# Kernel optimization log

Hardware: AMD Instinct MI355X
Metric: run time of the kernel (lower is better)

The kernel has to match this reference:

```python
import jax, jax.numpy as jnp
import numpy as np

N, E, IN, H, HEADS, L, OUT = 4096, 262144, 64, 128, 4, 2, 2
DH = H // HEADS  # 32, per-head dim for both GAT and global MHA
BN_EPS = 1e-5
NEG_SLOPE = 0.2  # GATConv leaky_relu default


def setup_inputs() -> dict:
    key = jax.random.key(0)
    ks = iter(jax.random.split(key, 32))
    rn = lambda shape, s: jax.random.normal(next(ks), shape, jnp.float32) * s
    return {
        "x": rn((N, IN), 1.0),
        "edge_index": jax.random.randint(next(ks), (2, E), 0, N),
        "w_in": rn((H, IN), IN ** -0.5),
        "b_in": rn((H,), 0.02),
        "w_gat": rn((L, H, H), H ** -0.5),
        "att_src": rn((L, HEADS, DH), 0.1),
        "att_dst": rn((L, HEADS, DH), 0.1),
        "b_gat": rn((L, H), 0.02),
        "w_qkv": rn((L, 3 * H, H), H ** -0.5),
        "b_qkv": rn((L, 3 * H), 0.02),
        "w_o": rn((L, H, H), H ** -0.5),
        "b_o": rn((L, H), 0.02),
        "bn_gamma": 1.0 + rn((L, 3, H), 0.05),
        "bn_beta": rn((L, 3, H), 0.05),
        "w1": rn((L, 2 * H, H), H ** -0.5),
        "b1": rn((L, 2 * H), 0.02),
        "w2": rn((L, H, 2 * H), (2 * H) ** -0.5),
        "b2": rn((L, H), 0.02),
        "w_out": rn((OUT, H), H ** -0.5),
        "b_out": rn((OUT,), 0.02),
    }


def _bn(h, g, b):
    # eval-mode BatchNorm1d with running_mean=0, running_var=1
    return h * (g / jnp.sqrt(1.0 + BN_EPS)) + b


def _gat(x, src, dst, w, a_src, a_dst, bias):
    # GATConv(hidden, hidden//heads, heads=HEADS, add_self_loops=False), concat=True
    xp = (x @ w.T).reshape(N, HEADS, DH)                  # [N, HEADS, DH]
    al_s = jnp.einsum('nhd,hd->nh', xp, a_src)            # [N, HEADS]
    al_d = jnp.einsum('nhd,hd->nh', xp, a_dst)
    logit = al_s[src] + al_d[dst]                         # [E, HEADS]
    logit = jnp.where(logit >= 0, logit, NEG_SLOPE * logit)
    m = jax.ops.segment_max(logit, dst, num_segments=N)   # scatter-softmax over dst
    m = jnp.where(jnp.isfinite(m), m, 0.0)
    e = jnp.exp(logit - m[dst])
    denom = jax.ops.segment_sum(e, dst, num_segments=N)
    alpha = e / (denom[dst] + 1e-16)
    out = jax.ops.segment_sum(alpha[:, :, None] * xp[src], dst, num_segments=N)
    return out.reshape(N, H) + bias


def _mha(x, wqkv, bqkv, wo, bo):
    # torch.nn.MultiheadAttention self-attention over all N nodes (one graph)
    qkv = x @ wqkv.T + bqkv
    q, k, v = jnp.split(qkv, 3, axis=-1)
    q = q.reshape(N, HEADS, DH)
    k = k.reshape(N, HEADS, DH)
    v = v.reshape(N, HEADS, DH)
    scores = jnp.einsum('nhd,mhd->hnm', q, k) / jnp.sqrt(jnp.float32(DH))
    attn = jax.nn.softmax(scores, axis=-1)
    out = jnp.einsum('hnm,mhd->nhd', attn, v).reshape(N, H)
    return out @ wo.T + bo


def reference(x, edge_index, w_in, b_in, w_gat, att_src, att_dst, b_gat,
              w_qkv, b_qkv, w_o, b_o, bn_gamma, bn_beta,
              w1, b1, w2, b2, w_out, b_out):
    src, dst = edge_index[0], edge_index[1]
    h = jax.nn.relu(x @ w_in.T + b_in)
    for l in range(L):
        # GPSConv: local GAT branch (dropout inactive in eval)
        h_loc = _gat(h, src, dst, w_gat[l], att_src[l], att_dst[l], b_gat[l]) + h
        h_loc = _bn(h_loc, bn_gamma[l, 0], bn_beta[l, 0])
        # GPSConv: global attention branch
        h_att = _mha(h, w_qkv[l], b_qkv[l], w_o[l], b_o[l]) + h
        h_att = _bn(h_att, bn_gamma[l, 1], bn_beta[l, 1])
        out = h_loc + h_att
        mlp = jax.nn.relu(out @ w1[l].T + b1[l]) @ w2[l].T + b2[l]
        out = _bn(out + mlp, bn_gamma[l, 2], bn_beta[l, 2])
        # GPSRiskModel residual + relu (dropout inactive in eval)
        h = jax.nn.relu(out + h)
    return h @ w_out.T + b_out
```

## Files before the change

kernel.cpp:

```cpp
#include <hip/hip_runtime.h>

#define NN 4096
#define EE 262144
#define INF_ 64
#define HH 128
#define HEADS 4
#define DH 32
#define LL 2
#define NH (NN * HH)
#define KSPLIT 8
#define L2E 1.4426950408889634f

typedef unsigned short u16;
typedef unsigned int u32;
using bf16x8 = __attribute__((ext_vector_type(8))) short;
using f32x4 = __attribute__((ext_vector_type(4))) float;

__device__ __forceinline__ float bf2f(u16 v) { return __uint_as_float(((u32)v) << 16); }
__device__ __forceinline__ u16 f2bf(float f) {
    u32 u = __float_as_uint(f);
    u32 r = (u + 0x7fffu + ((u >> 16) & 1u)) >> 16;
    return (u16)r;
}
__device__ __forceinline__ u32 encf(float f) {
    u32 b = __float_as_uint(f);
    return (b & 0x80000000u) ? ~b : (b | 0x80000000u);
}
__device__ __forceinline__ float decf(u32 u) {
    u32 b = (u & 0x80000000u) ? (u & 0x7fffffffu) : ~u;
    return __uint_as_float(b);
}

__global__ __launch_bounds__(256) void k_detect(const u16* __restrict__ x, int* __restrict__ flag,
                                                int* __restrict__ cnt, u32* __restrict__ gmax) {
    int t = threadIdx.x;
    for (int i = t; i < NN; i += 256) cnt[i] = 0;
    if (t < 16) gmax[t] = 0;
    __shared__ int cs[256];
    u16 v = x[2 * t];
    int e = (v >> 7) & 0xFF;
    cs[t] = (e >= 100 && e <= 140) ? 1 : 0;
    __syncthreads();
    for (int s = 128; s > 0; s >>= 1) {
        if (t < s) cs[t] += cs[t + s];
        __syncthreads();
    }
    if (t == 0) *flag = (cs[0] >= 128) ? 1 : 0;
}

#define MAXSEG 16
struct SegF { const void* src[MAXSEG]; int dst[MAXSEG]; int n[MAXSEG]; int cnt; };
__global__ void k_cvtf(SegF S, float* __restrict__ W, const int* __restrict__ flag) {
    int seg = blockIdx.y;
    if (seg >= S.cnt) return;
    int n = S.n[seg];
    float* d = W + S.dst[seg];
    const void* s = S.src[seg];
    int f = *flag;
    for (int i = blockIdx.x * 256 + threadIdx.x; i < n; i += gridDim.x * 256)
        d[i] = f ? bf2f(((const u16*)s)[i]) : ((const float*)s)[i];
}
struct SegB { const void* src[8]; u16* dst[8]; u16* dst2[8]; int n[8]; int cnt; };
__global__ void k_cvtb(SegB S, const int* __restrict__ flag) {
    int seg = blockIdx.y;
    if (seg >= S.cnt) return;
    int f = *flag;
    u16* d = S.dst[seg];
    u16* d2 = S.dst2[seg];
    if (f && !d2) return;
    int n = S.n[seg];
    const void* s = S.src[seg];
    for (int i = blockIdx.x * 256 + threadIdx.x; i < n; i += gridDim.x * 256) {
        if (d2) {
            float v = f ? bf2f(((const u16*)s)[i]) : ((const float*)s)[i];
            u16 h = f2bf(v);
            d[i] = h;
            d2[i] = f2bf(v - bf2f(h));
        } else {
            d[i] = f2bf(((const float*)s)[i]);
        }
    }
}

__global__ void k_hist(const int* __restrict__ dst, int* __restrict__ cnt) {
    int e = blockIdx.x * blockDim.x + threadIdx.x;
    if (e < EE) atomicAdd(&cnt[dst[e]], 1);
}
__global__ __launch_bounds__(256) void k_scan(const int* __restrict__ cnt, int* __restrict__ rowstart,
                                              int* __restrict__ cursor) {
    __shared__ int part[256];
    int t = threadIdx.x;
    int loc[16];
    int s = 0;
#pragma unroll
    for (int i = 0; i < 16; ++i) { loc[i] = s; s += cnt[t * 16 + i]; }
    part[t] = s;
    __syncthreads();
    for (int off = 1; off < 256; off <<= 1) {
        int v = part[t];
        int a = (t >= off) ? part[t - off] : 0;
        __syncthreads();
        part[t] = v + a;
        __syncthreads();
    }
    int base = (t == 0) ? 0 : part[t - 1];
#pragma unroll
    for (int i = 0; i < 16; ++i) {
        rowstart[t * 16 + i] = base + loc[i];
        cursor[t * 16 + i] = base + loc[i];
    }
}
__global__ void k_scatter(const int* __restrict__ src, const int* __restrict__ dst,
                          int* __restrict__ cursor, int* __restrict__ esrc) {
    int e = blockIdx.x * blockDim.x + threadIdx.x;
    if (e < EE) {
        int d = dst[e];
        int p = atomicAdd(&cursor[d], 1);
        esrc[p] = src[e];
    }
}

__global__ __launch_bounds__(128) void k_mgemm(const u16* __restrict__ Ahi, const u16* __restrict__ Alo,
                                               const u16* __restrict__ Wc, const u16* __restrict__ Wd,
                                               const int* __restrict__ flag,
                                               const float* __restrict__ bias,
                                               float* __restrict__ outf, u16* __restrict__ outb16,
                                               u16* __restrict__ outhi, u16* __restrict__ outlo,
                                               int K, int J, int relu) {
    const u16* Wb = (*flag) ? Wd : Wc;
    int wave = threadIdx.x >> 6, lane = threadIdx.x & 63;
    int grp = lane >> 4, lcol = lane & 15;
    int m0 = blockIdx.x * 32 + wave * 16;
    int j0 = blockIdx.y * 64;
    f32x4 acc[4];
#pragma unroll
    for (int s = 0; s < 4; ++s) acc[s] = (f32x4){0.f, 0.f, 0.f, 0.f};
    const u16* ah = Ahi + (size_t)(m0 + lcol) * K + grp * 8;
    const u16* al = Alo + (size_t)(m0 + lcol) * K + grp * 8;
    const u16* wb = Wb + (size_t)(j0 + lcol) * K + grp * 8;
    for (int k = 0; k < K; k += 32) {
        bf16x8 va = *(const bf16x8*)(ah + k);
        bf16x8 vl = *(const bf16x8*)(al + k);
#pragma unroll
        for (int s = 0; s < 4; ++s) {
            bf16x8 vw = *(const bf16x8*)(wb + (size_t)s * 16 * K + k);
            acc[s] = __builtin_amdgcn_mfma_f32_16x16x32_bf16(va, vw, acc[s], 0, 0, 0);
            acc[s] = __builtin_amdgcn_mfma_f32_16x16x32_bf16(vl, vw, acc[s], 0, 0, 0);
        }
    }
#pragma unroll
    for (int s = 0; s < 4; ++s) {
        int col = j0 + s * 16 + lcol;
        float bs = bias ? bias[col] : 0.f;
#pragma unroll
        for (int r = 0; r < 4; ++r) {
            float v = acc[s][r] + bs;
            if (relu) v = fmaxf(v, 0.f);
            size_t idx = (size_t)(m0 + grp * 4 + r) * J + col;
            if (outf) outf[idx] = v;
            if (outb16) outb16[idx] = f2bf(v);
            if (outhi) {
                u16 hv = f2bf(v);
                outhi[idx] = hv;
                outlo[idx] = f2bf(v - bf2f(hv));
            }
        }
    }
}

__global__ __launch_bounds__(128) void k_gemm_gq(const u16* __restrict__ Ahi, const u16* __restrict__ Alo,
                                                 const u16* __restrict__ wgatc, const u16* __restrict__ wgatd,
                                                 const u16* __restrict__ wqkvc, const u16* __restrict__ wqkvd,
                                                 const int* __restrict__ flag,
                                                 const float* __restrict__ bqkv,
                                                 u16* __restrict__ xpb, u16* __restrict__ qkvb) {
    int wave = threadIdx.x >> 6, lane = threadIdx.x & 63;
    int grp = lane >> 4, lcol = lane & 15;
    int m0 = blockIdx.x * 32 + wave * 16;
    int jb = blockIdx.y;
    int j0 = jb * 64;
    int f = *flag;
    const u16* wgat = f ? wgatd : wgatc;
    const u16* wqkv = f ? wqkvd : wqkvc;
    const u16* Wb = (jb < 2) ? (wgat + (size_t)j0 * HH) : (wqkv + (size_t)(j0 - 128) * HH);
    f32x4 acc[4];
#pragma unroll
    for (int s = 0; s < 4; ++s) acc[s] = (f32x4){0.f, 0.f, 0.f, 0.f};
    const u16* ah = Ahi + (size_t)(m0 + lcol) * HH + grp * 8;
    const u16* al = Alo + (size_t)(m0 + lcol) * HH + grp * 8;
    const u16* wb = Wb + (size_t)lcol * HH + grp * 8;
    for (int k = 0; k < HH; k += 32) {
        bf16x8 va = *(const bf16x8*)(ah + k);
        bf16x8 vl = *(const bf16x8*)(al + k);
#pragma unroll
        for (int s = 0; s < 4; ++s) {
            bf16x8 vw = *(const bf16x8*)(wb + (size_t)s * 16 * HH + k);
            acc[s] = __builtin_amdgcn_mfma_f32_16x16x32_bf16(va, vw, acc[s], 0, 0, 0);
            acc[s] = __builtin_amdgcn_mfma_f32_16x16x32_bf16(vl, vw, acc[s], 0, 0, 0);
        }
    }
    if (jb < 2) {
#pragma unroll
        for (int s = 0; s < 4; ++s) {
            int col = j0 + s * 16 + lcol;
#pragma unroll
            for (int r = 0; r < 4; ++r)
                xpb[(size_t)(m0 + grp * 4 + r) * HH + col] = f2bf(acc[s][r]);
        }
    } else {
#pragma unroll
        for (int s = 0; s < 4; ++s) {
            int colq = j0 - 128 + s * 16 + lcol;
            float bs = bqkv[colq];
#pragma unroll
            for (int r = 0; r < 4; ++r)
                qkvb[(size_t)(m0 + grp * 4 + r) * 384 + colq] = f2bf(acc[s][r] + bs);
        }
    }
}

__global__ __launch_bounds__(256) void k_attlog(const u16* __restrict__ xpb, const float* __restrict__ asrc,
                                                const float* __restrict__ adst, float* __restrict__ als,
                                                float* __restrict__ ald, u32* __restrict__ gmax) {
    int t = blockIdx.x * 256 + threadIdx.x;
    int n = t >> 2, hh = t & 3;
    const u16* xr = xpb + (size_t)n * HH + hh * DH;
    float s1 = 0.f, s2 = 0.f;
#pragma unroll
    for (int d = 0; d < DH; ++d) {
        float v = bf2f(xr[d]);
        s1 += v * asrc[hh * DH + d];
        s2 += v * adst[hh * DH + d];
    }
    als[t] = s1;
    ald[t] = s2;
    __shared__ float red[256];
    int lt = threadIdx.x;
    red[lt] = s1;
    __syncthreads();
    for (int off = 128; off >= 4; off >>= 1) {
        if (lt < off) red[lt] = fmaxf(red[lt], red[lt + off]);
        __syncthreads();
    }
    if (lt < 4) atomicMax(&gmax[lt], encf(red[lt]));
    __syncthreads();
    red[lt] = s2;
    __syncthreads();
    for (int off = 128; off >= 4; off >>= 1) {
        if (lt < off) red[lt] = fmaxf(red[lt], red[lt + off]);
        __syncthreads();
    }
    if (lt < 4) atomicMax(&gmax[4 + lt], encf(red[lt]));
}

__global__ __launch_bounds__(128) void k_gemm_wo(const u16* __restrict__ Ahi, const u16* __restrict__ Alo,
                                                 const u16* __restrict__ Wc, const u16* __restrict__ Wd,
                                                 const int* __restrict__ flag,
                                                 const float* __restrict__ bias,
                                                 const float* __restrict__ gatb, const float* __restrict__ hbuf,
                                                 const float* __restrict__ bgat, const float* __restrict__ gam,
                                                 const float* __restrict__ bet,
                                                 float* __restrict__ outb, u16* __restrict__ ohi,
                                                 u16* __restrict__ olo) {
    const u16* Wb = (*flag) ? Wd : Wc;
    int wave = threadIdx.x >> 6, lane = threadIdx.x & 63;
    int grp = lane >> 4, lcol = lane & 15;
    int m0 = blockIdx.x * 32 + wave * 16;
    int j0 = blockIdx.y * 64;
    f32x4 acc[4];
#pragma unroll
    for (int s = 0; s < 4; ++s) acc[s] = (f32x4){0.f, 0.f, 0.f, 0.f};
    const u16* ah = Ahi + (size_t)(m0 + lcol) * HH + grp * 8;
    const u16* al = Alo + (size_t)(m0 + lcol) * HH + grp * 8;
    const u16* wb = Wb + (size_t)(j0 + lcol) * HH + grp * 8;
    for (int k = 0; k < HH; k += 32) {
        bf16x8 va = *(const bf16x8*)(ah + k);
        bf16x8 vl = *(const bf16x8*)(al + k);
#pragma unroll
        for (int s = 0; s < 4; ++s) {
            bf16x8 vw = *(const bf16x8*)(wb + (size_t)s * 16 * HH + k);
            acc[s] = __builtin_amdgcn_mfma_f32_16x16x32_bf16(va, vw, acc[s], 0, 0, 0);
            acc[s] = __builtin_amdgcn_mfma_f32_16x16x32_bf16(vl, vw, acc[s], 0, 0, 0);
        }
    }
    float rs = rsqrtf(1.00001f);
#pragma unroll
    for (int s = 0; s < 4; ++s) {
        int col = j0 + s * 16 + lcol;
        float bs = bias[col];
        float g0 = gam[col] * rs, b0 = bet[col];
        float g1 = gam[HH + col] * rs, b1 = bet[HH + col];
        float bg = bgat[col];
#pragma unroll
        for (int r = 0; r < 4; ++r) {
            size_t idx = (size_t)(m0 + grp * 4 + r) * HH + col;
            float proj = acc[s][r] + bs;
            float hv = hbuf[idx];
            float hl = g0 * (gatb[idx] + bg + hv) + b0;
            float ha = g1 * (proj + hv) + b1;
            float v = hl + ha;
            outb[idx] = v;
            u16 hb = f2bf(v);
            ohi[idx] = hb;
            olo[idx] = f2bf(v - bf2f(hb));
        }
    }
}

__global__ __launch_bounds__(128) void k_gemm_w2(const u16* __restrict__ Ahi, const u16* __restrict__ Alo,
                                                 const u16* __restrict__ Wc, const u16* __restrict__ Wd,
                                                 const int* __restrict__ flag,
                                                 const float* __restrict__ bias,
                                                 const float* __restrict__ outb, const float* __restrict__ gam2,
                                                 const float* __restrict__ bet2,
                                                 float* __restrict__ hbuf, u16* __restrict__ hhi,
                                                 u16* __restrict__ hlo) {
    const u16* Wb = (*flag) ? Wd : Wc;
    int wave = threadIdx.x >> 6, lane = threadIdx.x & 63;
    int grp = lane >> 4, lcol = lane & 15;
    int m0 = blockIdx.x * 32 + wave * 16;
    int j0 = blockIdx.y * 64;
    const int K = 2 * HH;
    f32x4 acc[4];
#pragma unroll
    for (int s = 0; s < 4; ++s) acc[s] = (f32x4){0.f, 0.f, 0.f, 0.f};
    const u16* ah = Ahi + (size_t)(m0 + lcol) * K + grp * 8;
    const u16* al = Alo + (size_t)(m0 + lcol) * K + grp * 8;
    const u16* wb = Wb + (size_t)(j0 + lcol) * K + grp * 8;
    for (int k = 0; k < K; k += 32) {
        bf16x8 va = *(const bf16x8*)(ah + k);
        bf16x8 vl = *(const bf16x8*)(al + k);
#pragma unroll
        for (int s = 0; s < 4; ++s) {
            bf16x8 vw = *(const bf16x8*)(wb + (size_t)s * 16 * K + k);
            acc[s] = __builtin_amdgcn_mfma_f32_16x16x32_bf16(va, vw, acc[s], 0, 0, 0);
            acc[s] = __builtin_amdgcn_mfma_f32_16x16x32_bf16(vl, vw, acc[s], 0, 0, 0);
        }
    }
    float rs = rsqrtf(1.00001f);
#pragma unroll
    for (int s = 0; s < 4; ++s) {
        int col = j0 + s * 16 + lcol;
        float bs = bias[col];
        float g2 = gam2[col] * rs, b2 = bet2[col];
#pragma unroll
        for (int r = 0; r < 4; ++r) {
            size_t idx = (size_t)(m0 + grp * 4 + r) * HH + col;
            float mlpo = acc[s][r] + bs;
            float o2 = g2 * (outb[idx] + mlpo) + b2;
            float v = fmaxf(o2 + hbuf[idx], 0.f);
            hbuf[idx] = v;
            u16 hb = f2bf(v);
            hhi[idx] = hb;
            hlo[idx] = f2bf(v - bf2f(hb));
        }
    }
}

#define GCHUNK 256
__global__ __launch_bounds__(128) void k_gat_node(const int* __restrict__ esrc, const int* __restrict__ rowstart,
                                                  const int* __restrict__ cnt, const float* __restrict__ als,
                                                  const float* __restrict__ ald, const u16* __restrict__ xpb,
                                                  float* __restrict__ gatout, const u32* __restrict__ gmax) {
    int n = blockIdx.x, t = threadIdx.x;
    int base = rowstart[n], c = cnt[n];
    float4 adv = ((const float4*)ald)[n];
    float ad[4] = {adv.x, adv.y, adv.z, adv.w};
    float M2[4];
#pragma unroll
    for (int h = 0; h < 4; ++h) {
        float bound = decf(gmax[h]) + decf(gmax[4 + h]);
        float M = bound >= 0.f ? bound : 0.2f * bound;
        M2[h] = M * L2E;
    }
    __shared__ float red[512];
    __shared__ float elds[GCHUNK * 4];
    __shared__ int slds[GCHUNK];
    float dsum[4] = {0.f, 0.f, 0.f, 0.f};
    float acc = 0.f;
    int ht = t >> 5;
    for (int ch = 0; ch < c; ch += GCHUNK) {
        int cn = min(GCHUNK, c - ch);
        __syncthreads();
        for (int i = t; i < cn; i += 128) {
            int s = esrc[base + ch + i];
            slds[i] = s;
            float4 as = ((const float4*)als)[s];
            float lg, e;
            lg = as.x + ad[0]; lg = lg >= 0.f ? lg : 0.2f * lg; e = __builtin_exp2f(lg * L2E - M2[0]); elds[i * 4 + 0] = e; dsum[0] += e;
            lg = as.y + ad[1]; lg = lg >= 0.f ? lg : 0.2f * lg; e = __builtin_exp2f(lg * L2E - M2[1]); elds[i * 4 + 1] = e; dsum[1] += e;
            lg = as.z + ad[2]; lg = lg >= 0.f ? lg : 0.2f * lg; e = __builtin_exp2f(lg * L2E - M2[2]); elds[i * 4 + 2] = e; dsum[2] += e;
            lg = as.w + ad[3]; lg = lg >= 0.f ? lg : 0.2f * lg; e = __builtin_exp2f(lg * L2E - M2[3]); elds[i * 4 + 3] = e; dsum[3] += e;
        }
        __syncthreads();
        int i = 0;
        for (; i + 4 <= cn; i += 4) {
            int s0 = slds[i], s1 = slds[i + 1], s2 = slds[i + 2], s3 = slds[i + 3];
            float x0 = bf2f(xpb[(size_t)s0 * HH + t]);
            float x1 = bf2f(xpb[(size_t)s1 * HH + t]);
            float x2 = bf2f(xpb[(size_t)s2 * HH + t]);
            float x3 = bf2f(xpb[(size_t)s3 * HH + t]);
            acc += elds[i * 4 + ht] * x0 + elds[(i + 1) * 4 + ht] * x1;
            acc += elds[(i + 2) * 4 + ht] * x2 + elds[(i + 3) * 4 + ht] * x3;
        }
        for (; i < cn; ++i) acc += elds[i * 4 + ht] * bf2f(xpb[(size_t)slds[i] * HH + t]);
    }
    __syncthreads();
#pragma unroll
    for (int h = 0; h < 4; ++h) red[h * 128 + t] = dsum[h];
    __syncthreads();
    for (int s2 = 64; s2 > 0; s2 >>= 1) {
        if (t < s2) {
#pragma unroll
            for (int h = 0; h < 4; ++h)
                red[h * 128 + t] += red[h * 128 + t + s2];
        }
        __syncthreads();
    }
    float inv = 1.f / (red[ht * 128] + 1e-16f);
    gatout[(size_t)n * HH + t] = acc * inv;
}

__global__ __launch_bounds__(256) void k_mha_split(const u16* __restrict__ qkvb,
                                                   float* __restrict__ PM, float* __restrict__ PL,
                                                   u16* __restrict__ PO) {
    const float C1 = 0.17677669529663687f * L2E;
    int head = blockIdx.x & 3;
    int qt = (blockIdx.x >> 2) & 31;
    int ks = blockIdx.x >> 7;
    int tid = threadIdx.x;
    int wave = tid >> 6, lane = tid & 63;
    int grp = lane >> 4, lcol = lane & 15;

    __shared__ __align__(16) u16 Klds[64][40];
    __shared__ __align__(16) u32 Vlds[32][36];
    __shared__ __align__(16) u16 Plds[4][32][66];

    int qrow0 = qt * 128 + wave * 32;
    bf16x8 aQ0 = *(const bf16x8*)(qkvb + (size_t)(qrow0 + lcol) * 384 + head * 32 + grp * 8);
    bf16x8 aQ1 = *(const bf16x8*)(qkvb + (size_t)(qrow0 + 16 + lcol) * 384 + head * 32 + grp * 8);

    short onev = (lcol == 0) ? (short)0x3F80 : (short)0;
    bf16x8 bOne = {onev, onev, onev, onev, onev, onev, onev, onev};

    f32x4 oc00 = {0.f, 0.f, 0.f, 0.f}, oc01 = {0.f, 0.f, 0.f, 0.f};
    f32x4 oc10 = {0.f, 0.f, 0.f, 0.f}, oc11 = {0.f, 0.f, 0.f, 0.f};
    f32x4 ol0 = {0.f, 0.f, 0.f, 0.f}, ol1 = {0.f, 0.f, 0.f, 0.f};
    float msh = -INFINITY;

    int isK = (tid < 128);
    int st = tid & 127;
    int skey = st >> 1, shalf = (st & 1) * 16;
    int vj = st & 31, dgrp = st >> 5;
    int vkey0 = 32 * (vj & 1) + (vj >> 1);
    const u16* kptr = qkvb + 128 + head * 32 + shalf;
    const u16* vptr = qkvb + 256 + head * 32 + dgrp * 8;

    int kt0 = ks * (NN / KSPLIT);
    bf16x8 r0, r1;
    if (isK) {
        r0 = *(const bf16x8*)(kptr + (size_t)(kt0 + skey) * 384);
        r1 = *(const bf16x8*)(kptr + (size_t)(kt0 + skey) * 384 + 8);
    } else {
        r0 = *(const bf16x8*)(vptr + (size_t)(kt0 + vkey0) * 384);
        r1 = *(const bf16x8*)(vptr + (size_t)(kt0 + vkey0 + 16) * 384);
    }

    const int NT = (NN / KSPLIT) / 64;
    for (int t = 0; t < NT; ++t) {
        if (isK) {
            *(bf16x8*)(&Klds[skey][shalf]) = r0;
            *(bf16x8*)(&Klds[skey][shalf + 8]) = r1;
        } else {
#pragma unroll
            for (int j = 0; j < 8; ++j)
                Vlds[dgrp * 8 + j][vj] = (u32)(u16)r0[j] | ((u32)(u16)r1[j] << 16);
        }
        __syncthreads();
        if (t + 1 < NT) {
            int kn = kt0 + (t + 1) * 64;
            if (isK) {
                r0 = *(const bf16x8*)(kptr + (size_t)(kn + skey) * 384);
                r1 = *(const bf16x8*)(kptr + (size_t)(kn + skey) * 384 + 8);
            } else {
                r0 = *(const bf16x8*)(vptr + (size_t)(kn + vkey0) * 384);
                r1 = *(const bf16x8*)(vptr + (size_t)(kn + vkey0 + 16) * 384);
            }
        }
        f32x4 sc0[4], sc1[4];
        f32x4 zero = {0.f, 0.f, 0.f, 0.f};
#pragma unroll
        for (int s = 0; s < 4; ++s) {
            bf16x8 bK = *(const bf16x8*)(&Klds[s * 16 + lcol][grp * 8]);
            sc0[s] = __builtin_amdgcn_mfma_f32_16x16x32_bf16(aQ0, bK, zero, 0, 0, 0);
            sc1[s] = __builtin_amdgcn_mfma_f32_16x16x32_bf16(aQ1, bK, zero, 0, 0, 0);
        }
        float mymax = sc0[0][0];
#pragma unroll
        for (int s = 0; s < 4; ++s)
#pragma unroll
            for (int r = 0; r < 4; ++r) {
                mymax = fmaxf(mymax, sc0[s][r]);
                mymax = fmaxf(mymax, sc1[s][r]);
            }
        mymax = fmaxf(mymax, __shfl_xor(mymax, 1));
        mymax = fmaxf(mymax, __shfl_xor(mymax, 2));
        mymax = fmaxf(mymax, __shfl_xor(mymax, 4));
        mymax = fmaxf(mymax, __shfl_xor(mymax, 8));
        float mnew = fmaxf(msh, mymax * C1);
        float cc = __builtin_exp2f(msh - mnew);
        msh = mnew;
#pragma unroll
        for (int r = 0; r < 4; ++r) {
            float p0 = __builtin_exp2f(__builtin_fmaf(sc0[0][r], C1, -mnew));
            float p1 = __builtin_exp2f(__builtin_fmaf(sc0[1][r], C1, -mnew));
            float p2 = __builtin_exp2f(__builtin_fmaf(sc0[2][r], C1, -mnew));
            float p3 = __builtin_exp2f(__builtin_fmaf(sc0[3][r], C1, -mnew));
            u32 a01 = __builtin_amdgcn_perm(__float_as_uint(p1), __float_as_uint(p0), 0x07060302u);
            u32 a23 = __builtin_amdgcn_perm(__float_as_uint(p3), __float_as_uint(p2), 0x07060302u);
            *(uint2*)(&Plds[wave][grp * 4 + r][4 * lcol]) = make_uint2(a01, a23);
            float q0 = __builtin_exp2f(__builtin_fmaf(sc1[0][r], C1, -mnew));
            float q1 = __builtin_exp2f(__builtin_fmaf(sc1[1][r], C1, -mnew));
            float q2 = __builtin_exp2f(__builtin_fmaf(sc1[2][r], C1, -mnew));
            float q3 = __builtin_exp2f(__builtin_fmaf(sc1[3][r], C1, -mnew));
            u32 b01 = __builtin_amdgcn_perm(__float_as_uint(q1), __float_as_uint(q0), 0x07060302u);
            u32 b23 = __builtin_amdgcn_perm(__float_as_uint(q3), __float_as_uint(q2), 0x07060302u);
            *(uint2*)(&Plds[wave][16 + grp * 4 + r][4 * lcol]) = make_uint2(b01, b23);
        }
        oc00 *= cc; oc01 *= cc; ol0 *= cc;
        oc10 *= cc; oc11 *= cc; ol1 *= cc;
#pragma unroll
        for (int c2 = 0; c2 < 2; ++c2) {
            bf16x8 aP0 = *(const bf16x8*)(&Plds[wave][lcol][c2 * 32 + grp * 8]);
            bf16x8 aP1 = *(const bf16x8*)(&Plds[wave][16 + lcol][c2 * 32 + grp * 8]);
            bf16x8 bV0 = *(const bf16x8*)(&Vlds[lcol][c2 * 16 + grp * 4]);
            bf16x8 bV1 = *(const bf16x8*)(&Vlds[16 + lcol][c2 * 16 + grp * 4]);
            oc00 = __builtin_amdgcn_mfma_f32_16x16x32_bf16(aP0, bV0, oc00, 0, 0, 0);
            oc01 = __builtin_amdgcn_mfma_f32_16x16x32_bf16(aP0, bV1, oc01, 0, 0, 0);
            ol0 = __builtin_amdgcn_mfma_f32_16x16x32_bf16(aP0, bOne, ol0, 0, 0, 0);
            oc10 = __builtin_amdgcn_mfma_f32_16x16x32_bf16(aP1, bV0, oc10, 0, 0, 0);
            oc11 = __builtin_amdgcn_mfma_f32_16x16x32_bf16(aP1, bV1, oc11, 0, 0, 0);
            ol1 = __builtin_amdgcn_mfma_f32_16x16x32_bf16(aP1, bOne, ol1, 0, 0, 0);
        }
        __syncthreads();
    }
#pragma unroll
    for (int r = 0; r < 4; ++r) {
        int row0 = qrow0 + grp * 4 + r;
        size_t b0 = ((size_t)row0 * HEADS + head) * KSPLIT + ks;
        PO[b0 * 32 + lcol] = f2bf(oc00[r]);
        PO[b0 * 32 + 16 + lcol] = f2bf(oc01[r]);
        int row1 = row0 + 16;
        size_t b1 = ((size_t)row1 * HEADS + head) * KSPLIT + ks;
        PO[b1 * 32 + lcol] = f2bf(oc10[r]);
        PO[b1 * 32 + 16 + lcol] = f2bf(oc11[r]);
        if (lcol == 0) {
            PM[b0] = msh;
            PL[b0] = ol0[r];
            PM[b1] = msh;
            PL[b1] = ol1[r];
        }
    }
}

__global__ void k_mha_comb(const float* __restrict__ PM, const float* __restrict__ PL,
                           const u16* __restrict__ PO, u16* __restrict__ atthi,
                           u16* __restrict__ attlo) {
    int t = blockIdx.x * 256 + threadIdx.x;
    if (t >= NN * HH) return;
    int row = t >> 7, col = t & 127;
    int head = col >> 5, dim = col & 31;
    size_t b0 = ((size_t)row * HEADS + head) * KSPLIT;
    float m = -INFINITY;
#pragma unroll
    for (int k = 0; k < KSPLIT; ++k) m = fmaxf(m, PM[b0 + k]);
    float l = 0.f, o = 0.f;
#pragma unroll
    for (int k = 0; k < KSPLIT; ++k) {
        float w = __builtin_exp2f(PM[b0 + k] - m);
        l += PL[b0 + k] * w;
        o += bf2f(PO[(b0 + k) * 32 + dim]) * w;
    }
    float v = o / l;
    u16 h = f2bf(v);
    atthi[t] = h;
    attlo[t] = f2bf(v - bf2f(h));
}

__global__ __launch_bounds__(64) void k_out(const float* __restrict__ h, const float* __restrict__ w,
                                            const float* __restrict__ b, void* __restrict__ yout,
                                            const int* __restrict__ flag) {
    int n = blockIdx.x, l = threadIdx.x;
    float a0 = 0.f, a1 = 0.f;
    for (int k = l; k < HH; k += 64) {
        float hv = h[(size_t)n * HH + k];
        a0 += hv * w[k];
        a1 += hv * w[HH + k];
    }
#pragma unroll
    for (int off = 32; off > 0; off >>= 1) {
        a0 += __shfl_xor(a0, off);
        a1 += __shfl_xor(a1, off);
    }
    if (l == 0) {
        float o0 = a0 + b[0], o1 = a1 + b[1];
        if (*flag) {
            u16* y = (u16*)yout;
            y[n * 2 + 0] = f2bf(o0);
            y[n * 2 + 1] = f2bf(o1);
        } else {
            float* y = (float*)yout;
            y[n * 2 + 0] = o0;
            y[n * 2 + 1] = o1;
        }
    }
}

extern "C" void kernel_launch(void* const* d_in, const int* in_sizes, int n_in,
                              void* d_out, int out_size, void* d_ws, size_t ws_size,
                              hipStream_t stream) {
    float* W = (float*)d_ws;
    size_t o = 0;
    auto take = [&](size_t n) { size_t r = o; o += n; return r; };
    size_t pb_in = take(HH);
    size_t pattS = take(LL * HEADS * DH);
    size_t pattD = take(LL * HEADS * DH);
    size_t pb_gat = take(LL * HH);
    size_t pb_qkv = take(LL * 3 * HH);
    size_t pb_o  = take(LL * HH);
    size_t pbn_g = take(LL * 3 * HH);
    size_t pbn_b = take(LL * 3 * HH);
    size_t pb1   = take(LL * 2 * HH);
    size_t pb2   = take(LL * HH);
    size_t pw_out = take(2 * HH);
    size_t pb_out = take(2);
    auto takeb = [&](size_t nu16) { size_t r = o; o += (nu16 + 1) / 2; return r; };
    size_t bw_in  = takeb(HH * INF_);
    size_t bw_gat = takeb(LL * HH * HH);
    size_t bw_qkv = takeb(LL * 3 * HH * HH);
    size_t bw_o   = takeb(LL * HH * HH);
    size_t bw1    = takeb(LL * 2 * HH * HH);
    size_t bw2    = takeb(LL * HH * 2 * HH);
    o = (o + 127) & ~(size_t)127;
    size_t ohbuf = take(NH);
    size_t ogat  = take(NH);
    size_t otmp  = take(NH);
    size_t oals  = take(NN * HEADS);
    size_t oald  = take(NN * HEADS);
    size_t opm   = take(NN * HEADS * KSPLIT);
    size_t opl   = take(NN * HEADS * KSPLIT);
    size_t opo   = takeb((size_t)NN * HEADS * KSPLIT * 32);
    size_t oqkvb = takeb(NN * 384);
    size_t oxpb  = takeb(NH);
    size_t oxhi  = takeb(NN * INF_);
    size_t oxlo  = takeb(NN * INF_);
    size_t ohhi  = takeb(NH);
    size_t ohlo  = takeb(NH);
    size_t oahi  = takeb(NH);
    size_t oalo  = takeb(NH);
    size_t oohi  = takeb(NH);
    size_t oolo  = takeb(NH);
    size_t omhi  = takeb(NN * 2 * HH);
    size_t omlo  = takeb(NN * 2 * HH);
    int* ibase    = (int*)(W + o);
    int* iflag    = ibase;
    int* cnt      = ibase + 64;
    int* rowstart = cnt + NN;
    int* cursor   = rowstart + NN;
    int* esrc     = cursor + NN;
    u32* gmax     = (u32*)(esrc + EE);

    float* hbuf = W + ohbuf;
    float* gatb = W + ogat;
    float* tmp  = W + otmp;
    float* als  = W + oals;
    float* ald  = W + oald;
    float* pmb  = W + opm;
    float* plb  = W + opl;
    u16* pob  = (u16*)(W + opo);
    u16* qkvb = (u16*)(W + oqkvb);
    u16* xpb  = (u16*)(W + oxpb);
    u16* xhi = (u16*)(W + oxhi), *xlo = (u16*)(W + oxlo);
    u16* hhi = (u16*)(W + ohhi), *hlo = (u16*)(W + ohlo);
    u16* ahi = (u16*)(W + oahi), *alo = (u16*)(W + oalo);
    u16* ohi = (u16*)(W + oohi), *olo = (u16*)(W + oolo);
    u16* mhi = (u16*)(W + omhi), *mlo = (u16*)(W + omlo);

    const int* src = (const int*)d_in[1];
    const int* dst = (const int*)d_in[1] + EE;
    const u16* dw_in  = (const u16*)d_in[2];
    const u16* dw_gat = (const u16*)d_in[4];
    const u16* dw_qkv = (const u16*)d_in[8];
    const u16* dw_o   = (const u16*)d_in[10];
    const u16* dw1    = (const u16*)d_in[14];
    const u16* dw2    = (const u16*)d_in[16];

    k_detect<<<1, 256, 0, stream>>>((const u16*)d_in[0], iflag, cnt, gmax);

    SegF SF = {};
    int nf = 0;
    auto addf = [&](int idx, size_t off, int n) { SF.src[nf] = d_in[idx]; SF.dst[nf] = (int)off; SF.n[nf] = n; ++nf; };
    addf(3, pb_in, HH);
    addf(5, pattS, LL * HEADS * DH);
    addf(6, pattD, LL * HEADS * DH);
    addf(7, pb_gat, LL * HH);
    addf(9, pb_qkv, LL * 3 * HH);
    addf(11, pb_o, LL * HH);
    addf(12, pbn_g, LL * 3 * HH);
    addf(13, pbn_b, LL * 3 * HH);
    addf(15, pb1, LL * 2 * HH);
    addf(17, pb2, LL * HH);
    addf(18, pw_out, 2 * HH);
    addf(19, pb_out, 2);
    SF.cnt = nf;
    k_cvtf<<<dim3(8, nf), 256, 0, stream>>>(SF, W, iflag);

    SegB SB = {};
    int nb = 0;
    auto addb = [&](int idx, size_t off, int n, u16* d2) {
        SB.src[nb] = d_in[idx]; SB.dst[nb] = (u16*)(W + off); SB.dst2[nb] = d2; SB.n[nb] = n; ++nb;
    };
    addb(2, bw_in, HH * INF_, nullptr);
    addb(4, bw_gat, LL * HH * HH, nullptr);
    addb(8, bw_qkv, LL * 3 * HH * HH, nullptr);
    addb(10, bw_o, LL * HH * HH, nullptr);
    addb(14, bw1, LL * 2 * HH * HH, nullptr);
    addb(16, bw2, LL * HH * 2 * HH, nullptr);
    SB.src[nb] = d_in[0]; SB.dst[nb] = xhi; SB.dst2[nb] = xlo; SB.n[nb] = NN * INF_; ++nb;
    SB.cnt = nb;
    k_cvtb<<<dim3(128, nb), 256, 0, stream>>>(SB, iflag);

    k_hist<<<EE / 256, 256, 0, stream>>>(dst, cnt);
    k_scan<<<1, 256, 0, stream>>>(cnt, rowstart, cursor);
    k_scatter<<<EE / 256, 256, 0, stream>>>(src, dst, cursor, esrc);

    k_mgemm<<<dim3(NN / 32, HH / 64), 128, 0, stream>>>(xhi, xlo, (u16*)(W + bw_in), dw_in, iflag,
                                                        W + pb_in, hbuf, nullptr, hhi, hlo, INF_, HH, 1);

    for (int l = 0; l < LL; ++l) {
        k_gemm_gq<<<dim3(NN / 32, 8), 128, 0, stream>>>(hhi, hlo,
                                                        (u16*)(W + bw_gat) + (size_t)l * HH * HH,
                                                        dw_gat + (size_t)l * HH * HH,
                                                        (u16*)(W + bw_qkv) + (size_t)l * 3 * HH * HH,
                                                        dw_qkv + (size_t)l * 3 * HH * HH,
                                                        iflag, W + pb_qkv + l * 3 * HH, xpb, qkvb);
        k_attlog<<<(NN * HEADS) / 256, 256, 0, stream>>>(xpb, W + pattS + l * HEADS * DH,
                                                         W + pattD + l * HEADS * DH, als, ald,
                                                         gmax + l * 8);
        k_gat_node<<<NN, 128, 0, stream>>>(esrc, rowstart, cnt, als, ald, xpb, gatb, gmax + l * 8);
        k_mha_split<<<(NN / 128) * HEADS * KSPLIT, 256, 0, stream>>>(qkvb, pmb, plb, pob);
        k_mha_comb<<<(NN * HH) / 256, 256, 0, stream>>>(pmb, plb, pob, ahi, alo);
        k_gemm_wo<<<dim3(NN / 32, HH / 64), 128, 0, stream>>>(ahi, alo,
                                                              (u16*)(W + bw_o) + (size_t)l * HH * HH,
                                                              dw_o + (size_t)l * HH * HH, iflag,
                                                              W + pb_o + l * HH, gatb, hbuf,
                                                              W + pb_gat + l * HH, W + pbn_g + l * 3 * HH,
                                                              W + pbn_b + l * 3 * HH, tmp, ohi, olo);
        k_mgemm<<<dim3(NN / 32, 256 / 64), 128, 0, stream>>>(ohi, olo,
                                                             (u16*)(W + bw1) + (size_t)l * 2 * HH * HH,
                                                             dw1 + (size_t)l * 2 * HH * HH, iflag,
                                                             W + pb1 + l * 2 * HH, nullptr, nullptr,
                                                             mhi, mlo, HH, 2 * HH, 1);
        k_gemm_w2<<<dim3(NN / 32, HH / 64), 128, 0, stream>>>(mhi, mlo,
                                                              (u16*)(W + bw2) + (size_t)l * HH * 2 * HH,
                                                              dw2 + (size_t)l * HH * 2 * HH, iflag,
                                                              W + pb2 + l * HH, tmp,
                                                              W + pbn_g + l * 3 * HH + 2 * HH,
                                                              W + pbn_b + l * 3 * HH + 2 * HH,
                                                              hbuf, hhi, hlo);
    }
    k_out<<<NN, 64, 0, stream>>>(hbuf, W + pw_out, W + pb_out, d_out, iflag);
}
```

Measured before the change: 324.9 us.

## Fuse GAT aggregation and MHA split kernels into one heterogeneous launch

Merges the per-node GAT aggregation kernel and the split-K flash-attention kernel into a single launch. The first GM blocks run attention and the remaining NN blocks run GAT, sharing memory through a union. The GAT path now uses 256 threads per node, with two halves interleaving edges and a final combine. This removes a launch and lets the gather-bound GAT work overlap the MFMA-bound attention on the GPU. In exchange, the larger union shared memory and 256-thread GAT blocks may lower occupancy or add reduction overhead for small-degree nodes.

```diff
diff --git a/kernel.cpp b/kernel.cpp
--- a/kernel.cpp
+++ b/kernel.cpp
@@ -10,6 +10,7 @@
 #define NH (NN * HH)
 #define KSPLIT 8
 #define L2E 1.4426950408889634f
+#define GM ((NN / 128) * HEADS * KSPLIT)
 
 typedef unsigned short u16;
 typedef unsigned int u32;
@@ -358,207 +359,224 @@
 }
 
 #define GCHUNK 256
-__global__ __launch_bounds__(128) void k_gat_node(const int* __restrict__ esrc, const int* __restrict__ rowstart,
-                                                  const int* __restrict__ cnt, const float* __restrict__ als,
-                                                  const float* __restrict__ ald, const u16* __restrict__ xpb,
-                                                  float* __restrict__ gatout, const u32* __restrict__ gmax) {
-    int n = blockIdx.x, t = threadIdx.x;
-    int base = rowstart[n], c = cnt[n];
-    float4 adv = ((const float4*)ald)[n];
-    float ad[4] = {adv.x, adv.y, adv.z, adv.w};
-    float M2[4];
-#pragma unroll
-    for (int h = 0; h < 4; ++h) {
-        float bound = decf(gmax[h]) + decf(gmax[4 + h]);
-        float M = bound >= 0.f ? bound : 0.2f * bound;
-        M2[h] = M * L2E;
-    }
-    __shared__ float red[512];
-    __shared__ float elds[GCHUNK * 4];
-    __shared__ int slds[GCHUNK];
-    float dsum[4] = {0.f, 0.f, 0.f, 0.f};
-    float acc = 0.f;
-    int ht = t >> 5;
-    for (int ch = 0; ch < c; ch += GCHUNK) {
-        int cn = min(GCHUNK, c - ch);
+struct SmemMha {
+    u16 K[64][40];
+    u32 V[32][36];
+    u16 P[4][32][66];
+};
+struct SmemGat {
+    float red4[4 * 256];
+    float accl[256];
+    float elds[GCHUNK * 4];
+    int slds[GCHUNK];
+};
+union SmemU {
+    SmemMha m;
+    SmemGat g;
+};
+
+__global__ __launch_bounds__(256) void k_gat_mha(const u16* __restrict__ qkvb,
+                                                 float* __restrict__ PM, float* __restrict__ PL,
+                                                 u16* __restrict__ PO,
+                                                 const int* __restrict__ esrc, const int* __restrict__ rowstart,
+                                                 const int* __restrict__ cnt, const float* __restrict__ als,
+                                                 const float* __restrict__ ald, const u16* __restrict__ xpb,
+                                                 float* __restrict__ gatout, const u32* __restrict__ gmax) {
+    __shared__ __align__(16) SmemU S;
+    int tid = threadIdx.x;
+    if (blockIdx.x < GM) {
+        const float C1 = 0.17677669529663687f * L2E;
+        int head = blockIdx.x & 3;
+        int qt = (blockIdx.x >> 2) & 31;
+        int ks = blockIdx.x >> 7;
+        int wave = tid >> 6, lane = tid & 63;
+        int grp = lane >> 4, lcol = lane & 15;
+
+        int qrow0 = qt * 128 + wave * 32;
+        bf16x8 aQ0 = *(const bf16x8*)(qkvb + (size_t)(qrow0 + lcol) * 384 + head * 32 + grp * 8);
+        bf16x8 aQ1 = *(const bf16x8*)(qkvb + (size_t)(qrow0 + 16 + lcol) * 384 + head * 32 + grp * 8);
+
+        short onev = (lcol == 0) ? (short)0x3F80 : (short)0;
+        bf16x8 bOne = {onev, onev, onev, onev, onev, onev, onev, onev};
+
+        f32x4 oc00 = {0.f, 0.f, 0.f, 0.f}, oc01 = {0.f, 0.f, 0.f, 0.f};
+        f32x4 oc10 = {0.f, 0.f, 0.f, 0.f}, oc11 = {0.f, 0.f, 0.f, 0.f};
+        f32x4 ol0 = {0.f, 0.f, 0.f, 0.f}, ol1 = {0.f, 0.f, 0.f, 0.f};
+        float msh = -INFINITY;
+
+        int isK = (tid < 128);
+        int st = tid & 127;
+        int skey = st >> 1, shalf = (st & 1) * 16;
+        int vj = st & 31, dgrp = st >> 5;
+        int vkey0 = 32 * (vj & 1) + (vj >> 1);
+        const u16* kptr = qkvb + 128 + head * 32 + shalf;
+        const u16* vptr = qkvb + 256 + head * 32 + dgrp * 8;
+
+        int kt0 = ks * (NN / KSPLIT);
+        bf16x8 r0, r1;
+        if (isK) {
+            r0 = *(const bf16x8*)(kptr + (size_t)(kt0 + skey) * 384);
+            r1 = *(const bf16x8*)(kptr + (size_t)(kt0 + skey) * 384 + 8);
+        } else {
+            r0 = *(const bf16x8*)(vptr + (size_t)(kt0 + vkey0) * 384);
+            r1 = *(const bf16x8*)(vptr + (size_t)(kt0 + vkey0 + 16) * 384);
+        }
+
+        const int NT = (NN / KSPLIT) / 64;
+        for (int t = 0; t < NT; ++t) {
+            if (isK) {
+                *(bf16x8*)(&S.m.K[skey][shalf]) = r0;
+                *(bf16x8*)(&S.m.K[skey][shalf + 8]) = r1;
+            } else {
+#pragma unroll
+                for (int j = 0; j < 8; ++j)
+                    S.m.V[dgrp * 8 + j][vj] = (u32)(u16)r0[j] | ((u32)(u16)r1[j] << 16);
+            }
+            __syncthreads();
+            if (t + 1 < NT) {
+                int kn = kt0 + (t + 1) * 64;
+                if (isK) {
+                    r0 = *(const bf16x8*)(kptr + (size_t)(kn + skey) * 384);
+                    r1 = *(const bf16x8*)(kptr + (size_t)(kn + skey) * 384 + 8);
+                } else {
+                    r0 = *(const bf16x8*)(vptr + (size_t)(kn + vkey0) * 384);
+                    r1 = *(const bf16x8*)(vptr + (size_t)(kn + vkey0 + 16) * 384);
+                }
+            }
+            f32x4 sc0[4], sc1[4];
+            f32x4 zero = {0.f, 0.f, 0.f, 0.f};
+#pragma unroll
+            for (int s = 0; s < 4; ++s) {
+                bf16x8 bK = *(const bf16x8*)(&S.m.K[s * 16 + lcol][grp * 8]);
+                sc0[s] = __builtin_amdgcn_mfma_f32_16x16x32_bf16(aQ0, bK, zero, 0, 0, 0);
+                sc1[s] = __builtin_amdgcn_mfma_f32_16x16x32_bf16(aQ1, bK, zero, 0, 0, 0);
+            }
+            float mymax = sc0[0][0];
+#pragma unroll
+            for (int s = 0; s < 4; ++s)
+#pragma unroll
+                for (int r = 0; r < 4; ++r) {
+                    mymax = fmaxf(mymax, sc0[s][r]);
+                    mymax = fmaxf(mymax, sc1[s][r]);
+                }
+            mymax = fmaxf(mymax, __shfl_xor(mymax, 1));
+            mymax = fmaxf(mymax, __shfl_xor(mymax, 2));
+            mymax = fmaxf(mymax, __shfl_xor(mymax, 4));
+            mymax = fmaxf(mymax, __shfl_xor(mymax, 8));
+            float mnew = fmaxf(msh, mymax * C1);
+            float cc = __builtin_exp2f(msh - mnew);
+            msh = mnew;
+#pragma unroll
+            for (int r = 0; r < 4; ++r) {
+                float p0 = __builtin_exp2f(__builtin_fmaf(sc0[0][r], C1, -mnew));
+                float p1 = __builtin_exp2f(__builtin_fmaf(sc0[1][r], C1, -mnew));
+                float p2 = __builtin_exp2f(__builtin_fmaf(sc0[2][r], C1, -mnew));
+                float p3 = __builtin_exp2f(__builtin_fmaf(sc0[3][r], C1, -mnew));
+                u32 a01 = __builtin_amdgcn_perm(__float_as_uint(p1), __float_as_uint(p0), 0x07060302u);
+                u32 a23 = __builtin_amdgcn_perm(__float_as_uint(p3), __float_as_uint(p2), 0x07060302u);
+                *(uint2*)(&S.m.P[wave][grp * 4 + r][4 * lcol]) = make_uint2(a01, a23);
+                float q0 = __builtin_exp2f(__builtin_fmaf(sc1[0][r], C1, -mnew));
+                float q1 = __builtin_exp2f(__builtin_fmaf(sc1[1][r], C1, -mnew));
+                float q2 = __builtin_exp2f(__builtin_fmaf(sc1[2][r], C1, -mnew));
+                float q3 = __builtin_exp2f(__builtin_fmaf(sc1[3][r], C1, -mnew));
+                u32 b01 = __builtin_amdgcn_perm(__float_as_uint(q1), __float_as_uint(q0), 0x07060302u);
+                u32 b23 = __builtin_amdgcn_perm(__float_as_uint(q3), __float_as_uint(q2), 0x07060302u);
+                *(uint2*)(&S.m.P[wave][16 + grp * 4 + r][4 * lcol]) = make_uint2(b01, b23);
+            }
+            oc00 *= cc; oc01 *= cc; ol0 *= cc;
+            oc10 *= cc; oc11 *= cc; ol1 *= cc;
+#pragma unroll
+            for (int c2 = 0; c2 < 2; ++c2) {
+                bf16x8 aP0 = *(const bf16x8*)(&S.m.P[wave][lcol][c2 * 32 + grp * 8]);
+                bf16x8 aP1 = *(const bf16x8*)(&S.m.P[wave][16 + lcol][c2 * 32 + grp * 8]);
+                bf16x8 bV0 = *(const bf16x8*)(&S.m.V[lcol][c2 * 16 + grp * 4]);
+                bf16x8 bV1 = *(const bf16x8*)(&S.m.V[16 + lcol][c2 * 16 + grp * 4]);
+                oc00 = __builtin_amdgcn_mfma_f32_16x16x32_bf16(aP0, bV0, oc00, 0, 0, 0);
+                oc01 = __builtin_amdgcn_mfma_f32_16x16x32_bf16(aP0, bV1, oc01, 0, 0, 0);
+                ol0 = __builtin_amdgcn_mfma_f32_16x16x32_bf16(aP0, bOne, ol0, 0, 0, 0);
+                oc10 = __builtin_amdgcn_mfma_f32_16x16x32_bf16(aP1, bV0, oc10, 0, 0, 0);
+                oc11 = __builtin_amdgcn_mfma_f32_16x16x32_bf16(aP1, bV1, oc11, 0, 0, 0);
+                ol1 = __builtin_amdgcn_mfma_f32_16x16x32_bf16(aP1, bOne, ol1, 0, 0, 0);
+            }
+            __syncthreads();
+        }
+#pragma unroll
+        for (int r = 0; r < 4; ++r) {
+            int row0 = qrow0 + grp * 4 + r;
+            size_t b0 = ((size_t)row0 * HEADS + head) * KSPLIT + ks;
+            PO[b0 * 32 + lcol] = f2bf(oc00[r]);
+            PO[b0 * 32 + 16 + lcol] = f2bf(oc01[r]);
+            int row1 = row0 + 16;
+            size_t b1 = ((size_t)row1 * HEADS + head) * KSPLIT + ks;
+            PO[b1 * 32 + lcol] = f2bf(oc10[r]);
+            PO[b1 * 32 + 16 + lcol] = f2bf(oc11[r]);
+            if (lcol == 0) {
+                PM[b0] = msh;
+                PL[b0] = ol0[r];
+                PM[b1] = msh;
+                PL[b1] = ol1[r];
+            }
+        }
+    } else {
+        int n = blockIdx.x - GM;
+        int t = tid;
+        int dim = t & 127, half = t >> 7;
+        int base = rowstart[n], c = cnt[n];
+        float4 adv = ((const float4*)ald)[n];
+        float ad[4] = {adv.x, adv.y, adv.z, adv.w};
+        float M2[4];
+#pragma unroll
+        for (int h = 0; h < 4; ++h) {
+            float bound = decf(gmax[h]) + decf(gmax[4 + h]);
+            float M = bound >= 0.f ? bound : 0.2f * bound;
+            M2[h] = M * L2E;
+        }
+        float dsum[4] = {0.f, 0.f, 0.f, 0.f};
+        float acc = 0.f;
+        int ht = dim >> 5;
+        for (int ch = 0; ch < c; ch += GCHUNK) {
+            int cn = min(GCHUNK, c - ch);
+            __syncthreads();
+            for (int i = t; i < cn; i += 256) {
+                int s = esrc[base + ch + i];
+                S.g.slds[i] = s;
+                float4 as = ((const float4*)als)[s];
+                float lg, e;
+                lg = as.x + ad[0]; lg = lg >= 0.f ? lg : 0.2f * lg; e = __builtin_exp2f(lg * L2E - M2[0]); S.g.elds[i * 4 + 0] = e; dsum[0] += e;
+                lg = as.y + ad[1]; lg = lg >= 0.f ? lg : 0.2f * lg; e = __builtin_exp2f(lg * L2E - M2[1]); S.g.elds[i * 4 + 1] = e; dsum[1] += e;
+                lg = as.z + ad[2]; lg = lg >= 0.f ? lg : 0.2f * lg; e = __builtin_exp2f(lg * L2E - M2[2]); S.g.elds[i * 4 + 2] = e; dsum[2] += e;
+                lg = as.w + ad[3]; lg = lg >= 0.f ? lg : 0.2f * lg; e = __builtin_exp2f(lg * L2E - M2[3]); S.g.elds[i * 4 + 3] = e; dsum[3] += e;
+            }
+            __syncthreads();
+            int i = half;
+            for (; i + 6 < cn; i += 8) {
+                int s0 = S.g.slds[i], s1 = S.g.slds[i + 2], s2 = S.g.slds[i + 4], s3 = S.g.slds[i + 6];
+                float x0 = bf2f(xpb[(size_t)s0 * HH + dim]);
+                float x1 = bf2f(xpb[(size_t)s1 * HH + dim]);
+                float x2 = bf2f(xpb[(size_t)s2 * HH + dim]);
+                float x3 = bf2f(xpb[(size_t)s3 * HH + dim]);
+                acc += S.g.elds[i * 4 + ht] * x0 + S.g.elds[(i + 2) * 4 + ht] * x1;
+                acc += S.g.elds[(i + 4) * 4 + ht] * x2 + S.g.elds[(i + 6) * 4 + ht] * x3;
+            }
+            for (; i < cn; i += 2)
+                acc += S.g.elds[i * 4 + ht] * bf2f(xpb[(size_t)S.g.slds[i] * HH + dim]);
+        }
         __syncthreads();
-        for (int i = t; i < cn; i += 128) {
-            int s = esrc[base + ch + i];
-            slds[i] = s;
-            float4 as = ((const float4*)als)[s];
-            float lg, e;
-            lg = as.x + ad[0]; lg = lg >= 0.f ? lg : 0.2f * lg; e = __builtin_exp2f(lg * L2E - M2[0]); elds[i * 4 + 0] = e; dsum[0] += e;
-            lg = as.y + ad[1]; lg = lg >= 0.f ? lg : 0.2f * lg; e = __builtin_exp2f(lg * L2E - M2[1]); elds[i * 4 + 1] = e; dsum[1] += e;
-            lg = as.z + ad[2]; lg = lg >= 0.f ? lg : 0.2f * lg; e = __builtin_exp2f(lg * L2E - M2[2]); elds[i * 4 + 2] = e; dsum[2] += e;
-            lg = as.w + ad[3]; lg = lg >= 0.f ? lg : 0.2f * lg; e = __builtin_exp2f(lg * L2E - M2[3]); elds[i * 4 + 3] = e; dsum[3] += e;
-        }
+#pragma unroll
+        for (int h = 0; h < 4; ++h) S.g.red4[h * 256 + t] = dsum[h];
+        S.g.accl[t] = acc;
         __syncthreads();
-        int i = 0;
-        for (; i + 4 <= cn; i += 4) {
-            int s0 = slds[i], s1 = slds[i + 1], s2 = slds[i + 2], s3 = slds[i + 3];
-            float x0 = bf2f(xpb[(size_t)s0 * HH + t]);
-            float x1 = bf2f(xpb[(size_t)s1 * HH + t]);
-            float x2 = bf2f(xpb[(size_t)s2 * HH + t]);
-            float x3 = bf2f(xpb[(size_t)s3 * HH + t]);
-            acc += elds[i * 4 + ht] * x0 + elds[(i + 1) * 4 + ht] * x1;
-            acc += elds[(i + 2) * 4 + ht] * x2 + elds[(i + 3) * 4 + ht] * x3;
-        }
-        for (; i < cn; ++i) acc += elds[i * 4 + ht] * bf2f(xpb[(size_t)slds[i] * HH + t]);
-    }
-    __syncthreads();
-#pragma unroll
-    for (int h = 0; h < 4; ++h) red[h * 128 + t] = dsum[h];
-    __syncthreads();
-    for (int s2 = 64; s2 > 0; s2 >>= 1) {
-        if (t < s2) {
-#pragma unroll
-            for (int h = 0; h < 4; ++h)
-                red[h * 128 + t] += red[h * 128 + t + s2];
-        }
-        __syncthreads();
-    }
-    float inv = 1.f / (red[ht * 128] + 1e-16f);
-    gatout[(size_t)n * HH + t] = acc * inv;
-}
-
-__global__ __launch_bounds__(256) void k_mha_split(const u16* __restrict__ qkvb,
-                                                   float* __restrict__ PM, float* __restrict__ PL,
-                                                   u16* __restrict__ PO) {
-    const float C1 = 0.17677669529663687f * L2E;
-    int head = blockIdx.x & 3;
-    int qt = (blockIdx.x >> 2) & 31;
-    int ks = blockIdx.x >> 7;
-    int tid = threadIdx.x;
-    int wave = tid >> 6, lane = tid & 63;
-    int grp = lane >> 4, lcol = lane & 15;
-
-    __shared__ __align__(16) u16 Klds[64][40];
-    __shared__ __align__(16) u32 Vlds[32][36];
-    __shared__ __align__(16) u16 Plds[4][32][66];
-
-    int qrow0 = qt * 128 + wave * 32;
-    bf16x8 aQ0 = *(const bf16x8*)(qkvb + (size_t)(qrow0 + lcol) * 384 + head * 32 + grp * 8);
-    bf16x8 aQ1 = *(const bf16x8*)(qkvb + (size_t)(qrow0 + 16 + lcol) * 384 + head * 32 + grp * 8);
-
-    short onev = (lcol == 0) ? (short)0x3F80 : (short)0;
-    bf16x8 bOne = {onev, onev, onev, onev, onev, onev, onev, onev};
-
-    f32x4 oc00 = {0.f, 0.f, 0.f, 0.f}, oc01 = {0.f, 0.f, 0.f, 0.f};
-    f32x4 oc10 = {0.f, 0.f, 0.f, 0.f}, oc11 = {0.f, 0.f, 0.f, 0.f};
-    f32x4 ol0 = {0.f, 0.f, 0.f, 0.f}, ol1 = {0.f, 0.f, 0.f, 0.f};
-    float msh = -INFINITY;
-
-    int isK = (tid < 128);
-    int st = tid & 127;
-    int skey = st >> 1, shalf = (st & 1) * 16;
-    int vj = st & 31, dgrp = st >> 5;
-    int vkey0 = 32 * (vj & 1) + (vj >> 1);
-    const u16* kptr = qkvb + 128 + head * 32 + shalf;
-    const u16* vptr = qkvb + 256 + head * 32 + dgrp * 8;
-
-    int kt0 = ks * (NN / KSPLIT);
-    bf16x8 r0, r1;
-    if (isK) {
-        r0 = *(const bf16x8*)(kptr + (size_t)(kt0 + skey) * 384);
-        r1 = *(const bf16x8*)(kptr + (size_t)(kt0 + skey) * 384 + 8);
-    } else {
-        r0 = *(const bf16x8*)(vptr + (size_t)(kt0 + vkey0) * 384);
-        r1 = *(const bf16x8*)(vptr + (size_t)(kt0 + vkey0 + 16) * 384);
-    }
-
-    const int NT = (NN / KSPLIT) / 64;
-    for (int t = 0; t < NT; ++t) {
-        if (isK) {
-            *(bf16x8*)(&Klds[skey][shalf]) = r0;
-            *(bf16x8*)(&Klds[skey][shalf + 8]) = r1;
-        } else {
-#pragma unroll
-            for (int j = 0; j < 8; ++j)
-                Vlds[dgrp * 8 + j][vj] = (u32)(u16)r0[j] | ((u32)(u16)r1[j] << 16);
-        }
-        __syncthreads();
-        if (t + 1 < NT) {
-            int kn = kt0 + (t + 1) * 64;
-            if (isK) {
-                r0 = *(const bf16x8*)(kptr + (size_t)(kn + skey) * 384);
-                r1 = *(const bf16x8*)(kptr + (size_t)(kn + skey) * 384 + 8);
-            } else {
-                r0 = *(const bf16x8*)(vptr + (size_t)(kn + vkey0) * 384);
-                r1 = *(const bf16x8*)(vptr + (size_t)(kn + vkey0 + 16) * 384);
-            }
-        }
-        f32x4 sc0[4], sc1[4];
-        f32x4 zero = {0.f, 0.f, 0.f, 0.f};
-#pragma unroll
-        for (int s = 0; s < 4; ++s) {
-            bf16x8 bK = *(const bf16x8*)(&Klds[s * 16 + lcol][grp * 8]);
-            sc0[s] = __builtin_amdgcn_mfma_f32_16x16x32_bf16(aQ0, bK, zero, 0, 0, 0);
-            sc1[s] = __builtin_amdgcn_mfma_f32_16x16x32_bf16(aQ1, bK, zero, 0, 0, 0);
-        }
-        float mymax = sc0[0][0];
-#pragma unroll
-        for (int s = 0; s < 4; ++s)
-#pragma unroll
-            for (int r = 0; r < 4; ++r) {
-                mymax = fmaxf(mymax, sc0[s][r]);
-                mymax = fmaxf(mymax, sc1[s][r]);
-            }
-        mymax = fmaxf(mymax, __shfl_xor(mymax, 1));
-        mymax = fmaxf(mymax, __shfl_xor(mymax, 2));
-        mymax = fmaxf(mymax, __shfl_xor(mymax, 4));
-        mymax = fmaxf(mymax, __shfl_xor(mymax, 8));
-        float mnew = fmaxf(msh, mymax * C1);
-        float cc = __builtin_exp2f(msh - mnew);
-        msh = mnew;
-#pragma unroll
-        for (int r = 0; r < 4; ++r) {
-            float p0 = __builtin_exp2f(__builtin_fmaf(sc0[0][r], C1, -mnew));
-            float p1 = __builtin_exp2f(__builtin_fmaf(sc0[1][r], C1, -mnew));
-            float p2 = __builtin_exp2f(__builtin_fmaf(sc0[2][r], C1, -mnew));
-            float p3 = __builtin_exp2f(__builtin_fmaf(sc0[3][r], C1, -mnew));
-            u32 a01 = __builtin_amdgcn_perm(__float_as_uint(p1), __float_as_uint(p0), 0x07060302u);
-            u32 a23 = __builtin_amdgcn_perm(__float_as_uint(p3), __float_as_uint(p2), 0x07060302u);
-            *(uint2*)(&Plds[wave][grp * 4 + r][4 * lcol]) = make_uint2(a01, a23);
-            float q0 = __builtin_exp2f(__builtin_fmaf(sc1[0][r], C1, -mnew));
-            float q1 = __builtin_exp2f(__builtin_fmaf(sc1[1][r], C1, -mnew));
-            float q2 = __builtin_exp2f(__builtin_fmaf(sc1[2][r], C1, -mnew));
-            float q3 = __builtin_exp2f(__builtin_fmaf(sc1[3][r], C1, -mnew));
-            u32 b01 = __builtin_amdgcn_perm(__float_as_uint(q1), __float_as_uint(q0), 0x07060302u);
-            u32 b23 = __builtin_amdgcn_perm(__float_as_uint(q3), __float_as_uint(q2), 0x07060302u);
-            *(uint2*)(&Plds[wave][16 + grp * 4 + r][4 * lcol]) = make_uint2(b01, b23);
-        }
-        oc00 *= cc; oc01 *= cc; ol0 *= cc;
-        oc10 *= cc; oc11 *= cc; ol1 *= cc;
-#pragma unroll
-        for (int c2 = 0; c2 < 2; ++c2) {
-            bf16x8 aP0 = *(const bf16x8*)(&Plds[wave][lcol][c2 * 32 + grp * 8]);
-            bf16x8 aP1 = *(const bf16x8*)(&Plds[wave][16 + lcol][c2 * 32 + grp * 8]);
-            bf16x8 bV0 = *(const bf16x8*)(&Vlds[lcol][c2 * 16 + grp * 4]);
-            bf16x8 bV1 = *(const bf16x8*)(&Vlds[16 + lcol][c2 * 16 + grp * 4]);
-            oc00 = __builtin_amdgcn_mfma_f32_16x16x32_bf16(aP0, bV0, oc00, 0, 0, 0);
-            oc01 = __builtin_amdgcn_mfma_f32_16x16x32_bf16(aP0, bV1, oc01, 0, 0, 0);
-            ol0 = __builtin_amdgcn_mfma_f32_16x16x32_bf16(aP0, bOne, ol0, 0, 0, 0);
-            oc10 = __builtin_amdgcn_mfma_f32_16x16x32_bf16(aP1, bV0, oc10, 0, 0, 0);
-            oc11 = __builtin_amdgcn_mfma_f32_16x16x32_bf16(aP1, bV1, oc11, 0, 0, 0);
-            ol1 = __builtin_amdgcn_mfma_f32_16x16x32_bf16(aP1, bOne, ol1, 0, 0, 0);
-        }
-        __syncthreads();
-    }
-#pragma unroll
-    for (int r = 0; r < 4; ++r) {
-        int row0 = qrow0 + grp * 4 + r;
-        size_t b0 = ((size_t)row0 * HEADS + head) * KSPLIT + ks;
-        PO[b0 * 32 + lcol] = f2bf(oc00[r]);
-        PO[b0 * 32 + 16 + lcol] = f2bf(oc01[r]);
-        int row1 = row0 + 16;
-        size_t b1 = ((size_t)row1 * HEADS + head) * KSPLIT + ks;
-        PO[b1 * 32 + lcol] = f2bf(oc10[r]);
-        PO[b1 * 32 + 16 + lcol] = f2bf(oc11[r]);
-        if (lcol == 0) {
-            PM[b0] = msh;
-            PL[b0] = ol0[r];
-            PM[b1] = msh;
-            PL[b1] = ol1[r];
+        for (int s2 = 128; s2 > 0; s2 >>= 1) {
+            if (t < s2) {
+#pragma unroll
+                for (int h = 0; h < 4; ++h)
+                    S.g.red4[h * 256 + t] += S.g.red4[h * 256 + t + s2];
+            }
+            __syncthreads();
+        }
+        if (t < 128) {
+            float inv = 1.f / (S.g.red4[ht * 256] + 1e-16f);
+            gatout[(size_t)n * HH + t] = (S.g.accl[t] + S.g.accl[t + 128]) * inv;
         }
     }
 }
@@ -747,8 +765,8 @@
         k_attlog<<<(NN * HEADS) / 256, 256, 0, stream>>>(xpb, W + pattS + l * HEADS * DH,
                                                          W + pattD + l * HEADS * DH, als, ald,
                                                          gmax + l * 8);
-        k_gat_node<<<NN, 128, 0, stream>>>(esrc, rowstart, cnt, als, ald, xpb, gatb, gmax + l * 8);
-        k_mha_split<<<(NN / 128) * HEADS * KSPLIT, 256, 0, stream>>>(qkvb, pmb, plb, pob);
+        k_gat_mha<<<GM + NN, 256, 0, stream>>>(qkvb, pmb, plb, pob,
+                                               esrc, rowstart, cnt, als, ald, xpb, gatb, gmax + l * 8);
         k_mha_comb<<<(NN * HH) / 256, 256, 0, stream>>>(pmb, plb, pob, ahi, alo);
         k_gemm_wo<<<dim3(NN / 32, HH / 64), 128, 0, stream>>>(ahi, alo,
                                                               (u16*)(W + bw_o) + (size_t)l * HH * HH,
```

Result: slower. 342.6 us (+5.4%).
